# Kernel optimization log

Hardware: AMD Instinct MI355X
Metric: run time of the kernel (lower is better)

Reference implementation:

```python
import jax, jax.numpy as jnp
import numpy as np

B = 8192

def setup_inputs() -> dict:
    key = jax.random.key(0)
    k1, k2, k3 = jax.random.split(key, 3)
    z = jax.random.normal(k1, (B, 1), dtype=jnp.float32)
    censorship = jax.random.bernoulli(k2, 0.5, (B,)).astype(jnp.float32)
    times = jax.random.uniform(k3, (B,), dtype=jnp.float32) * 100.0
    c_t = jnp.stack([censorship, times], axis=1)  # (B, 2)
    return {"z": z, "c_t": c_t}

def reference(z, c_t):
    # phi='sigmoid', reduction='mean'
    censorship = c_t[:, 0]
    times = c_t[:, 1]
    events = 1.0 - censorship  # 1 if event observed
    zf = z[:, 0]  # (B,)
    # pair (a,b) comparable iff time_a < time_b and event_a observed;
    # then a is more risky, b less risky -> r = z_a - z_b
    comparable = (times[:, None] < times[None, :]) & (events[:, None] > 0)  # (B,B)
    r = zf[:, None] - zf[None, :]  # (B,B)
    vals = jnp.where(comparable, jax.nn.sigmoid(r), 0.0)
    n_pairs = jnp.sum(comparable)
    total = jnp.sum(vals)
    # mean over comparable pairs; return 0 if none (matches torch.zeros(1) fallback)
    loss = -jnp.where(n_pairs > 0, total / jnp.maximum(n_pairs, 1).astype(vals.dtype), 0.0)
    return loss
```

## Files before the change

kernel.cpp:

```cpp
#include <hip/hip_runtime.h>


constexpr int THREADS = 256;
constexpr int JT = 256;

__global__ __launch_bounds__(256) void surv_pairs(
    const float* __restrict__ z, const float* __restrict__ ct,
    float2* __restrict__ P, int njc)
{
    __shared__ float s_t[JT];
    __shared__ float s_e[JT];
    __shared__ float s_tg[THREADS];
    __shared__ float s_ri[THREADS];
    __shared__ int   s_wcnt[4];
    __shared__ float wsum[4];
    __shared__ int   wcnt2[4];

    const int tid = threadIdx.x;
    const int ib  = blockIdx.x / njc;
    const int jc  = blockIdx.x % njc;
    const int j0  = jc * JT;

    {
        const int j = j0 + tid;
        s_t[tid] = ct[2 * j + 1];
        s_e[tid] = __expf(z[j]);
    }

    const int i = ib * THREADS + tid;
    const float cens = ct[2 * i];
    const float ti   = ct[2 * i + 1];
    const float rii  = __expf(-z[i]);
    const bool  ev   = (1.0f - cens) > 0.0f;
    const unsigned long long mask = __ballot(ev);
    const int lane = tid & 63;
    const int wid  = tid >> 6;
    if (lane == 0) s_wcnt[wid] = __popcll(mask);
    __syncthreads();
    int base = 0;
    for (int w = 0; w < wid; ++w) base += s_wcnt[w];
    const int m = s_wcnt[0] + s_wcnt[1] + s_wcnt[2] + s_wcnt[3];
    const int pos = base + __popcll(mask & ((1ull << lane) - 1ull));
    if (ev) { s_tg[pos] = ti; s_ri[pos] = rii; }
    __syncthreads();

    const int chunk = (wid + (int)blockIdx.x) & 3;
    const int row   = chunk * 64 + lane;
    const bool act  = row < m;
    const float tg = act ? s_tg[row] : __builtin_inff();
    const float ri = act ? s_ri[row] : 0.0f;

    float fsum = 0.0f;
    int   cnt  = 0;
    if (chunk * 64 < m) {
        const float4* t4 = reinterpret_cast<const float4*>(s_t);
        const float4* e4 = reinterpret_cast<const float4*>(s_e);
#pragma unroll 8
        for (int q = 0; q < JT / 4; ++q) {
            const float4 t = t4[q];
            const float4 e = e4[q];
            { bool c = tg < t.x; float d = __builtin_fmaf(e.x, ri, 1.0f); float s = __builtin_amdgcn_rcpf(d); fsum += c ? s : 0.0f; cnt += c; }
            { bool c = tg < t.y; float d = __builtin_fmaf(e.y, ri, 1.0f); float s = __builtin_amdgcn_rcpf(d); fsum += c ? s : 0.0f; cnt += c; }
            { bool c = tg < t.z; float d = __builtin_fmaf(e.z, ri, 1.0f); float s = __builtin_amdgcn_rcpf(d); fsum += c ? s : 0.0f; cnt += c; }
            { bool c = tg < t.w; float d = __builtin_fmaf(e.w, ri, 1.0f); float s = __builtin_amdgcn_rcpf(d); fsum += c ? s : 0.0f; cnt += c; }
        }
    }

    for (int off = 32; off > 0; off >>= 1) {
        fsum += __shfl_down(fsum, off);
        cnt  += __shfl_down(cnt, off);
    }
    if (lane == 0) { wsum[wid] = fsum; wcnt2[wid] = cnt; }
    __syncthreads();
    if (tid == 0) {
        const float bs = wsum[0] + wsum[1] + wsum[2] + wsum[3];
        const int   bc = wcnt2[0] + wcnt2[1] + wcnt2[2] + wcnt2[3];
        P[blockIdx.x] = make_float2(bs, (float)bc);
    }
}

__global__ __launch_bounds__(64) void surv_fin(
    const float2* __restrict__ P, int nb, float* __restrict__ out)
{
    const int lane = threadIdx.x;
    double s = 0.0, c = 0.0;
    for (int k = lane; k < nb; k += 64) {
        const float2 p = P[k];
        s += p.x; c += p.y;
    }
    for (int off = 32; off > 0; off >>= 1) {
        s += __shfl_down(s, off);
        c += __shfl_down(c, off);
    }
    if (lane == 0)
        out[0] = (c > 0.0) ? (float)(-(s / c)) : 0.0f;
}

extern "C" void kernel_launch(void* const* d_in, const int* in_sizes, int n_in,
                              void* d_out, int out_size, void* d_ws, size_t ws_size,
                              hipStream_t stream)
{
    const float* z  = (const float*)d_in[0];
    const float* ct = (const float*)d_in[1];
    float* out = (float*)d_out;
    const int B = in_sizes[0];

    const int NB  = B / THREADS;
    const int njc = B / JT;

    float2* P = (float2*)d_ws;

    surv_pairs<<<NB * njc, THREADS, 0, stream>>>(z, ct, P, njc);
    surv_fin<<<1, 64, 0, stream>>>(P, NB * njc, out);
}
```

Baseline: 21.38 us.

## Fuse final reduction into pair kernel via last-block spin-wait on tagged slots

Merges the separate finalize kernel into the main pair kernel. Each block publishes its partial sum and count with a release store plus a per-slot magic tag. The last block spins on the tags and reduces all partials in double precision. This removes a second kernel launch and its launch gap. In exchange, correctness depends on the last block being able to wait for all others, which risks deadlock if blocks are not all resident. It also risks a stale match if the workspace already holds the same tags from a previous call.

Result: slower. 29.28 us (+36.9%).

```diff
diff --git a/kernel.cpp b/kernel.cpp
--- a/kernel.cpp
+++ b/kernel.cpp
@@ -4,9 +4,15 @@
 constexpr int THREADS = 256;
 constexpr int JT = 256;
 
-__global__ __launch_bounds__(256) void surv_pairs(
+__device__ __forceinline__ unsigned long long slot_magic(int k) {
+    return 0x51BE5EEDCAFEF00DULL ^ ((unsigned long long)k * 0x9E3779B97F4A7C15ULL);
+}
+
+__global__ __launch_bounds__(256) void surv_all(
     const float* __restrict__ z, const float* __restrict__ ct,
-    float2* __restrict__ P, int njc)
+    unsigned long long* __restrict__ Pd,
+    unsigned long long* __restrict__ Pt,
+    float* __restrict__ out, int njc)
 {
     __shared__ float s_t[JT];
     __shared__ float s_e[JT];
@@ -15,6 +21,8 @@
     __shared__ int   s_wcnt[4];
     __shared__ float wsum[4];
     __shared__ int   wcnt2[4];
+    __shared__ double ss[THREADS];
+    __shared__ double sc[THREADS];
 
     const int tid = threadIdx.x;
     const int ib  = blockIdx.x / njc;
@@ -73,27 +81,34 @@
     if (lane == 0) { wsum[wid] = fsum; wcnt2[wid] = cnt; }
     __syncthreads();
     if (tid == 0) {
-        const float bs = wsum[0] + wsum[1] + wsum[2] + wsum[3];
-        const int   bc = wcnt2[0] + wcnt2[1] + wcnt2[2] + wcnt2[3];
-        P[blockIdx.x] = make_float2(bs, (float)bc);
+        const float2 val = make_float2(wsum[0] + wsum[1] + wsum[2] + wsum[3],
+                                       (float)(wcnt2[0] + wcnt2[1] + wcnt2[2] + wcnt2[3]));
+        const unsigned long long bits = __builtin_bit_cast(unsigned long long, val);
+        __hip_atomic_store(&Pd[blockIdx.x], bits, __ATOMIC_RELEASE, __HIP_MEMORY_SCOPE_AGENT);
+        __hip_atomic_store(&Pt[blockIdx.x], slot_magic(blockIdx.x), __ATOMIC_RELEASE, __HIP_MEMORY_SCOPE_AGENT);
     }
-}
 
-__global__ __launch_bounds__(64) void surv_fin(
-    const float2* __restrict__ P, int nb, float* __restrict__ out)
-{
-    const int lane = threadIdx.x;
-    double s = 0.0, c = 0.0;
-    for (int k = lane; k < nb; k += 64) {
-        const float2 p = P[k];
-        s += p.x; c += p.y;
+    if (blockIdx.x == (unsigned)(gridDim.x - 1)) {
+        const int nb = (int)gridDim.x;
+        double s = 0.0, c = 0.0;
+        for (int k = tid; k < nb; k += THREADS) {
+            while (__hip_atomic_load(&Pt[k], __ATOMIC_ACQUIRE, __HIP_MEMORY_SCOPE_AGENT)
+                   != slot_magic(k))
+                __builtin_amdgcn_s_sleep(1);
+            const unsigned long long bits =
+                __hip_atomic_load(&Pd[k], __ATOMIC_RELAXED, __HIP_MEMORY_SCOPE_AGENT);
+            const float2 p = __builtin_bit_cast(float2, bits);
+            s += p.x; c += p.y;
+        }
+        ss[tid] = s; sc[tid] = c;
+        __syncthreads();
+        for (int off = THREADS / 2; off > 0; off >>= 1) {
+            if (tid < off) { ss[tid] += ss[tid + off]; sc[tid] += sc[tid + off]; }
+            __syncthreads();
+        }
+        if (tid == 0)
+            out[0] = (sc[0] > 0.0) ? (float)(-(ss[0] / sc[0])) : 0.0f;
     }
-    for (int off = 32; off > 0; off >>= 1) {
-        s += __shfl_down(s, off);
-        c += __shfl_down(c, off);
-    }
-    if (lane == 0)
-        out[0] = (c > 0.0) ? (float)(-(s / c)) : 0.0f;
 }
 
 extern "C" void kernel_launch(void* const* d_in, const int* in_sizes, int n_in,
@@ -107,9 +122,10 @@
 
     const int NB  = B / THREADS;
     const int njc = B / JT;
+    const int nb  = NB * njc;
 
-    float2* P = (float2*)d_ws;
+    unsigned long long* Pd = (unsigned long long*)d_ws;
+    unsigned long long* Pt = Pd + nb;
 
-    surv_pairs<<<NB * njc, THREADS, 0, stream>>>(z, ct, P, njc);
-    surv_fin<<<1, 64, 0, stream>>>(P, NB * njc, out);
+    surv_all<<<nb, THREADS, 0, stream>>>(z, ct, Pd, Pt, out, njc);
 }
```

## Hold two j columns per thread in registers and loop over compacted event rows

Applied to the files above, without the earlier changes.

Flips the pair-loop mapping. Each thread now keeps two j elements (time and exp(z)) in registers, and the loop runs over only the m event rows compacted into shared memory, read as broadcasts. This removes the shared-memory staging of the j tile and skips work for non-event rows without needing per-wave chunk guards. It also halves the block count to 16 j-tiles of 512 per i-block. The count is now taken with a wave ballot/popcount instead of per-lane accumulation, which adds scalar work per iteration and a data-dependent loop trip count.

Result: slower. 22.67 us (+6.0%).

```diff
diff --git a/kernel.cpp b/kernel.cpp
--- a/kernel.cpp
+++ b/kernel.cpp
@@ -2,14 +2,11 @@
 
 
 constexpr int THREADS = 256;
-constexpr int JT = 256;
 
 __global__ __launch_bounds__(256) void surv_pairs(
     const float* __restrict__ z, const float* __restrict__ ct,
-    float2* __restrict__ P, int njc)
+    float2* __restrict__ P)
 {
-    __shared__ float s_t[JT];
-    __shared__ float s_e[JT];
     __shared__ float s_tg[THREADS];
     __shared__ float s_ri[THREADS];
     __shared__ int   s_wcnt[4];
@@ -17,15 +14,14 @@
     __shared__ int   wcnt2[4];
 
     const int tid = threadIdx.x;
-    const int ib  = blockIdx.x / njc;
-    const int jc  = blockIdx.x % njc;
-    const int j0  = jc * JT;
+    const int ib  = blockIdx.x >> 4;
+    const int jr  = blockIdx.x & 15;
+    const int j0  = jr * 512 + tid * 2;
 
-    {
-        const int j = j0 + tid;
-        s_t[tid] = ct[2 * j + 1];
-        s_e[tid] = __expf(z[j]);
-    }
+    const float4 a  = *reinterpret_cast<const float4*>(&ct[2 * j0]);
+    const float tj0 = a.y, tj1 = a.w;
+    const float2 zz = *reinterpret_cast<const float2*>(&z[j0]);
+    const float ej0 = __expf(zz.x), ej1 = __expf(zz.y);
 
     const int i = ib * THREADS + tid;
     const float cens = ct[2 * i];
@@ -44,38 +40,33 @@
     if (ev) { s_tg[pos] = ti; s_ri[pos] = rii; }
     __syncthreads();
 
-    const int chunk = (wid + (int)blockIdx.x) & 3;
-    const int row   = chunk * 64 + lane;
-    const bool act  = row < m;
-    const float tg = act ? s_tg[row] : __builtin_inff();
-    const float ri = act ? s_ri[row] : 0.0f;
-
     float fsum = 0.0f;
-    int   cnt  = 0;
-    if (chunk * 64 < m) {
-        const float4* t4 = reinterpret_cast<const float4*>(s_t);
-        const float4* e4 = reinterpret_cast<const float4*>(s_e);
-#pragma unroll 8
-        for (int q = 0; q < JT / 4; ++q) {
-            const float4 t = t4[q];
-            const float4 e = e4[q];
-            { bool c = tg < t.x; float d = __builtin_fmaf(e.x, ri, 1.0f); float s = __builtin_amdgcn_rcpf(d); fsum += c ? s : 0.0f; cnt += c; }
-            { bool c = tg < t.y; float d = __builtin_fmaf(e.y, ri, 1.0f); float s = __builtin_amdgcn_rcpf(d); fsum += c ? s : 0.0f; cnt += c; }
-            { bool c = tg < t.z; float d = __builtin_fmaf(e.z, ri, 1.0f); float s = __builtin_amdgcn_rcpf(d); fsum += c ? s : 0.0f; cnt += c; }
-            { bool c = tg < t.w; float d = __builtin_fmaf(e.w, ri, 1.0f); float s = __builtin_amdgcn_rcpf(d); fsum += c ? s : 0.0f; cnt += c; }
+    int   scnt = 0;
+#pragma unroll 4
+    for (int k = 0; k < m; ++k) {
+        const float tg = s_tg[k];
+        const float ri = s_ri[k];
+        {
+            const bool  c = tg < tj0;
+            const float s = __builtin_amdgcn_rcpf(__builtin_fmaf(ej0, ri, 1.0f));
+            fsum += c ? s : 0.0f;
+            scnt += (int)__popcll(__ballot(c));
+        }
+        {
+            const bool  c = tg < tj1;
+            const float s = __builtin_amdgcn_rcpf(__builtin_fmaf(ej1, ri, 1.0f));
+            fsum += c ? s : 0.0f;
+            scnt += (int)__popcll(__ballot(c));
         }
     }
 
-    for (int off = 32; off > 0; off >>= 1) {
-        fsum += __shfl_down(fsum, off);
-        cnt  += __shfl_down(cnt, off);
-    }
-    if (lane == 0) { wsum[wid] = fsum; wcnt2[wid] = cnt; }
+    for (int off = 32; off > 0; off >>= 1) fsum += __shfl_down(fsum, off);
+    if (lane == 0) { wsum[wid] = fsum; wcnt2[wid] = scnt; }
     __syncthreads();
     if (tid == 0) {
-        const float bs = wsum[0] + wsum[1] + wsum[2] + wsum[3];
-        const int   bc = wcnt2[0] + wcnt2[1] + wcnt2[2] + wcnt2[3];
-        P[blockIdx.x] = make_float2(bs, (float)bc);
+        P[blockIdx.x] = make_float2(
+            wsum[0] + wsum[1] + wsum[2] + wsum[3],
+            (float)(wcnt2[0] + wcnt2[1] + wcnt2[2] + wcnt2[3]));
     }
 }
 
@@ -105,11 +96,10 @@
     float* out = (float*)d_out;
     const int B = in_sizes[0];
 
-    const int NB  = B / THREADS;
-    const int njc = B / JT;
+    const int nb = (B / THREADS) * 16;
 
     float2* P = (float2*)d_ws;
 
-    surv_pairs<<<NB * njc, THREADS, 0, stream>>>(z, ct, P, njc);
-    surv_fin<<<1, 64, 0, stream>>>(P, NB * njc, out);
+    surv_pairs<<<nb, THREADS, 0, stream>>>(z, ct, P);
+    surv_fin<<<1, 64, 0, stream>>>(P, nb, out);
 }
```
